# Kernel optimization log

Measured on AMD Instinct MI355X. Metric: run time of the kernel, lower is better.

Reference implementation:

```python
import jax, jax.numpy as jnp
import numpy as np

D_MODEL = 1024
N_HEADS = 16
HEAD_DIM = D_MODEL // N_HEADS


def setup_inputs() -> dict:
    key = jax.random.key(0)
    k1, k2, k3 = jax.random.split(key, 3)
    B, T = 4, 2048
    x = jax.random.normal(k1, (B, T, D_MODEL), dtype=jnp.float32)
    # match nn.Linear default init scale roughly (small weights for stability)
    w_qkv = jax.random.normal(k2, (D_MODEL, 3 * D_MODEL), dtype=jnp.float32) / np.sqrt(D_MODEL)
    w_proj = jax.random.normal(k3, (D_MODEL, D_MODEL), dtype=jnp.float32) / np.sqrt(D_MODEL)
    b_proj = jnp.zeros((D_MODEL,), dtype=jnp.float32)
    return {"x": x, "w_qkv": w_qkv, "w_proj": w_proj, "b_proj": b_proj}


def reference(x, w_qkv, w_proj, b_proj):
    B, T, C = x.shape
    qkv = x @ w_qkv  # [B,T,3C]
    q, k, v = jnp.split(qkv, 3, axis=-1)
    # [B, H, T, hd]
    q = q.reshape(B, T, N_HEADS, HEAD_DIM).transpose(0, 2, 1, 3)
    k = k.reshape(B, T, N_HEADS, HEAD_DIM).transpose(0, 2, 1, 3)
    v = v.reshape(B, T, N_HEADS, HEAD_DIM).transpose(0, 2, 1, 3)
    scale = 1.0 / np.sqrt(HEAD_DIM).astype(np.float32)
    att = jnp.einsum("bhqd,bhkd->bhqk", q, k) * scale
    causal = jnp.tril(jnp.ones((T, T), dtype=bool))
    att = jnp.where(causal[None, None], att, jnp.float32(-jnp.inf))
    att = jax.nn.softmax(att, axis=-1)
    # dropout p=0.0 (eval) -> identity
    out = jnp.einsum("bhqk,bhkd->bhqd", att, v)
    out = out.transpose(0, 2, 1, 3).reshape(B, T, C)
    return out @ w_proj + b_proj
```

## Files before the change

kernel.cpp:

```cpp
#include <hip/hip_runtime.h>
#include <stdint.h>

#define D_MODEL 1024
#define N_HEADS 16
#define HEAD_DIM 64
#define BATCH 4
#define SEQ 2048
#define ROWS (BATCH * SEQ)
#define K3 (3 * D_MODEL)
#define NQT (SEQ / 64)
#define SCALE_Q 0.1803368867f

typedef unsigned short u16;
typedef unsigned int u32;
typedef __attribute__((ext_vector_type(8))) short short8;
typedef __attribute__((ext_vector_type(4))) float floatx4;

typedef const __attribute__((address_space(1))) u32* gptr_t;
typedef __attribute__((address_space(3))) u32* lptr_t;

__device__ __forceinline__ unsigned cvt_pk(float lo, float hi) {
    unsigned r;
    asm("v_cvt_pk_bf16_f32 %0, %1, %2" : "=v"(r) : "v"(lo), "v"(hi));
    return r;
}

__global__ __launch_bounds__(256) void conv_f2b4(const float* __restrict__ x,
                                                 u16* __restrict__ xb, int n4) {
    int i = blockIdx.x * 256 + threadIdx.x;
    if (i < n4) {
        float4 v = ((const float4*)x)[i];
        uint2 p;
        p.x = cvt_pk(v.x, v.y);
        p.y = cvt_pk(v.z, v.w);
        ((uint2*)xb)[i] = p;
    }
}

__global__ __launch_bounds__(256) void transpose_f2b_t(const float* __restrict__ w,
                                                       u16* __restrict__ wt,
                                                       int R, int C) {
    __shared__ u16 tile[64][65];
    const int tx = threadIdx.x & 63;
    const int ty = threadIdx.x >> 6;
    const int r0 = blockIdx.y * 64, c0 = blockIdx.x * 64;
    #pragma unroll
    for (int i = 0; i < 16; i += 2) {
        const float a = w[(size_t)(r0 + i * 4 + ty) * C + c0 + tx];
        const float b = w[(size_t)(r0 + (i + 1) * 4 + ty) * C + c0 + tx];
        const unsigned p = cvt_pk(a, b);
        tile[i * 4 + ty][tx] = (u16)p;
        tile[(i + 1) * 4 + ty][tx] = (u16)(p >> 16);
    }
    __syncthreads();
    #pragma unroll
    for (int i = 0; i < 16; ++i) {
        const int c = i * 4 + ty;
        wt[(size_t)(c0 + c) * R + r0 + tx] = tile[tx][c];
    }
}

__global__ __launch_bounds__(256) void transpose_v2(const u16* __restrict__ v,
                                                    u16* __restrict__ vt) {
    __shared__ u16 tile[64][65];
    const int bh = blockIdx.y;
    const int t0 = blockIdx.x * 64;
    const int tx = threadIdx.x & 63, ty = threadIdx.x >> 6;
    const u16* src = v + ((size_t)bh * SEQ + t0) * HEAD_DIM;
    #pragma unroll
    for (int i = 0; i < 16; ++i) {
        const int r = i * 4 + ty;
        tile[r][tx] = src[r * HEAD_DIM + tx];
    }
    __syncthreads();
    u16* dst = vt + (size_t)bh * HEAD_DIM * SEQ + t0;
    #pragma unroll
    for (int i = 0; i < 16; ++i) {
        const int d = i * 4 + ty;
        dst[(size_t)d * SEQ + tx] = tile[tx][d];
    }
}

#define GEMM_CORE_GLD(KDIM, NXB)                                               \
    __shared__ u16 As[128][64];                                                \
    __shared__ u16 Bs[128][64];                                                \
    const int tid  = threadIdx.x;                                              \
    const int wave = tid >> 6, lane = tid & 63;                                \
    const int quad = lane >> 4, l15 = lane & 15;                               \
    const int wr = wave >> 1, wc = wave & 1;                                   \
    const int bid = (int)(blockIdx.y * gridDim.x + blockIdx.x);                \
    const int nwg = (int)(gridDim.x * gridDim.y);                              \
    const int swz = (bid & 7) * (nwg >> 3) + (bid >> 3);      \
    const int m0 = (swz / (NXB)) * 128, n0 = (swz % (NXB)) * 128;              \
    const int lrow8 = lane >> 3;                                               \
    const int csw = 8 * ((lane & 7) ^ lrow8);           \
    const int swA = (l15 & 7) * 8;                      \
    floatx4 acc[4][4] = {};                                                    \
    for (int k0 = 0; k0 < (KDIM); k0 += 64) {                                  \
        _Pragma("unroll")                                                      \
        for (int i = 0; i < 4; ++i) {                                          \
            const int rb = i * 32 + wave * 8;                                  \
            const int r  = rb + lrow8;                                         \
            __builtin_amdgcn_global_load_lds(                                  \
                (gptr_t)(A + (size_t)(m0 + r) * (KDIM) + k0 + csw),            \
                (lptr_t)(&As[rb][0]), 16, 0, 0);                               \
            __builtin_amdgcn_global_load_lds(                                  \
                (gptr_t)(Bt + (size_t)(n0 + r) * (KDIM) + k0 + csw),           \
                (lptr_t)(&Bs[rb][0]), 16, 0, 0);                               \
        }                                                                      \
        __syncthreads();                                                       \
        _Pragma("unroll")                                                      \
        for (int ks = 0; ks < 2; ++ks) {                                       \
            const int kk = ks * 32 + quad * 8;                                 \
            short8 af[4], bf[4];                                               \
            _Pragma("unroll")                                                  \
            for (int t = 0; t < 4; ++t) {                                      \
                af[t] = *(const short8*)&As[wr * 64 + t * 16 + l15][kk ^ swA]; \
                bf[t] = *(const short8*)&Bs[wc * 64 + t * 16 + l15][kk ^ swA]; \
            }                                                                  \
            _Pragma("unroll")                                                  \
            for (int i = 0; i < 4; ++i)                                        \
                _Pragma("unroll")                                              \
                for (int j = 0; j < 4; ++j)                                    \
                    acc[i][j] = __builtin_amdgcn_mfma_f32_16x16x32_bf16(       \
                        af[i], bf[j], acc[i][j], 0, 0, 0);                     \
        }                                                                      \
        __syncthreads();                                                       \
    }

__global__ __launch_bounds__(256) void gemm_qkv(const u16* __restrict__ A,
                                                const u16* __restrict__ Bt,
                                                u16* __restrict__ qo,
                                                u16* __restrict__ ko,
                                                u16* __restrict__ vo) {
    GEMM_CORE_GLD(D_MODEL, 24)
    const int which = n0 >> 10;
    u16* dst = which == 0 ? qo : (which == 1 ? ko : vo);
    const float scl = which == 0 ? SCALE_Q : 1.f;
    #pragma unroll
    for (int i = 0; i < 4; ++i)
        #pragma unroll
        for (int j = 0; j < 4; ++j) {
            const int col = n0 + wc * 64 + j * 16 + l15;
            const int rb  = m0 + wr * 64 + i * 16 + quad * 4;
            const int cc  = col & 1023;
            const int h = cc >> 6, d = cc & 63;
            #pragma unroll
            for (int rr = 0; rr < 4; rr += 2) {
                const unsigned pw = cvt_pk(acc[i][j][rr] * scl,
                                           acc[i][j][rr + 1] * scl);
                int row = rb + rr;
                int b_ = row >> 11, t_ = row & 2047;
                dst[(((size_t)(b_ * N_HEADS + h)) * SEQ + t_) * HEAD_DIM + d] =
                    (u16)pw;
                row = rb + rr + 1;
                b_ = row >> 11; t_ = row & 2047;
                dst[(((size_t)(b_ * N_HEADS + h)) * SEQ + t_) * HEAD_DIM + d] =
                    (u16)(pw >> 16);
            }
        }
}

__global__ __launch_bounds__(256) void gemm_proj(const u16* __restrict__ A,
                                                 const u16* __restrict__ Bt,
                                                 const float* __restrict__ bias,
                                                 float* __restrict__ out) {
    GEMM_CORE_GLD(D_MODEL, 8)
    #pragma unroll
    for (int i = 0; i < 4; ++i)
        #pragma unroll
        for (int j = 0; j < 4; ++j) {
            const int col = n0 + wc * 64 + j * 16 + l15;
            const int rb  = m0 + wr * 64 + i * 16 + quad * 4;
            const float bv = bias[col];
            #pragma unroll
            for (int rr = 0; rr < 4; ++rr) {
                const int row = rb + rr;
                out[(size_t)row * D_MODEL + col] = acc[i][j][rr] + bv;
            }
        }
}

__global__ __launch_bounds__(256, 4) void attn_mfma(const u16* __restrict__ q,
                                                    const u16* __restrict__ k,
                                                    const u16* __restrict__ vt,
                                                    u16* __restrict__ o) {
    __shared__ u16 Ks[2][64][64];
    __shared__ u16 Vs[2][64][64];
    __shared__ u16 Plds[4][16][64];
    const int tid = threadIdx.x;
    const int w = tid >> 6, lane = tid & 63;
    const int quad = lane >> 4, l15 = lane & 15;
    const int bid = (int)(blockIdx.y * 16 + blockIdx.x);
    const int swzb = (bid & 7) * 128 + (bid >> 3);
    const int bh = swzb >> 4;
    const int qx = swzb & 15;
    const int b = bh >> 4, h = bh & 15;
    const u16* kb  = k  + (size_t)bh * SEQ * HEAD_DIM;
    const u16* vtb = vt + (size_t)bh * HEAD_DIM * SEQ;
    const int lrow8 = lane >> 3;
    const int csw = 8 * ((lane & 7) ^ lrow8);
    const int swA = (l15 & 7) * 8;
    const int r0 = w * 16 + lrow8;
    const short8 ones = {0x3F80, 0x3F80, 0x3F80, 0x3F80,
                         0x3F80, 0x3F80, 0x3F80, 0x3F80};

    #pragma unroll 1
    for (int seg = 0; seg < 2; ++seg) {
        const int qt = seg ? qx : (NQT - 1 - qx);
        const int qrow = qt * 64 + w * 16 + l15;
        const u16* qp = q + ((size_t)bh * SEQ + qrow) * HEAD_DIM + quad * 8;
        const short8 bq0 = *(const short8*)(qp);
        const short8 bq1 = *(const short8*)(qp + 32);

        floatx4 O[4] = {};
        floatx4 Lacc = {};

        __syncthreads();
        __builtin_amdgcn_global_load_lds(
            (gptr_t)(kb + (size_t)(r0) * HEAD_DIM + csw),
            (lptr_t)(&Ks[0][w * 16][0]), 16, 0, 0);
        __builtin_amdgcn_global_load_lds(
            (gptr_t)(kb + (size_t)(r0 + 8) * HEAD_DIM + csw),
            (lptr_t)(&Ks[0][w * 16 + 8][0]), 16, 0, 0);
        __builtin_amdgcn_global_load_lds(
            (gptr_t)(vtb + (size_t)(r0) * SEQ + csw),
            (lptr_t)(&Vs[0][w * 16][0]), 16, 0, 0);
        __builtin_amdgcn_global_load_lds(
            (gptr_t)(vtb + (size_t)(r0 + 8) * SEQ + csw),
            (lptr_t)(&Vs[0][w * 16 + 8][0]), 16, 0, 0);

        for (int c = 0; c <= qt; ++c) {
            const int cb = c & 1;
            __syncthreads();
            if (c < qt) {
                const int nb = cb ^ 1;
                __builtin_amdgcn_global_load_lds(
                    (gptr_t)(kb + (size_t)((c + 1) * 64 + r0) * HEAD_DIM + csw),
                    (lptr_t)(&Ks[nb][w * 16][0]), 16, 0, 0);
                __builtin_amdgcn_global_load_lds(
                    (gptr_t)(kb + (size_t)((c + 1) * 64 + r0 + 8) * HEAD_DIM + csw),
                    (lptr_t)(&Ks[nb][w * 16 + 8][0]), 16, 0, 0);
                __builtin_amdgcn_global_load_lds(
                    (gptr_t)(vtb + (size_t)(r0) * SEQ + (c + 1) * 64 + csw),
                    (lptr_t)(&Vs[nb][w * 16][0]), 16, 0, 0);
                __builtin_amdgcn_global_load_lds(
                    (gptr_t)(vtb + (size_t)(r0 + 8) * SEQ + (c + 1) * 64 + csw),
                    (lptr_t)(&Vs[nb][w * 16 + 8][0]), 16, 0, 0);
            }
            floatx4 s[4];
            #pragma unroll
            for (int kt = 0; kt < 4; ++kt) {
                short8 ak0 = *(const short8*)&Ks[cb][kt * 16 + l15][(quad * 8) ^ swA];
                short8 ak1 = *(const short8*)&Ks[cb][kt * 16 + l15][(32 + quad * 8) ^ swA];
                floatx4 z = {};
                z = __builtin_amdgcn_mfma_f32_16x16x32_bf16(ak0, bq0, z, 0, 0, 0);
                z = __builtin_amdgcn_mfma_f32_16x16x32_bf16(ak1, bq1, z, 0, 0, 0);
                s[kt] = z;
            }
            float e[4][4];
            #pragma unroll
            for (int kt = 0; kt < 4; ++kt)
                #pragma unroll
                for (int r = 0; r < 4; ++r)
                    e[kt][r] = exp2f(s[kt][r]);
            if (c == qt) {
                #pragma unroll
                for (int kt = 0; kt < 4; ++kt)
                    #pragma unroll
                    for (int r = 0; r < 4; ++r)
                        if (kt * 16 + quad * 4 + r > w * 16 + l15) e[kt][r] = 0.f;
            }
            #pragma unroll
            for (int kt = 0; kt < 4; ++kt) {
                uint2 pkv;
                pkv.x = cvt_pk(e[kt][0], e[kt][1]);
                pkv.y = cvt_pk(e[kt][2], e[kt][3]);
                *(uint2*)&Plds[w][l15][(kt * 16 + quad * 4) ^ swA] = pkv;
            }
            short8 pb0 = *(const short8*)&Plds[w][l15][(quad * 8) ^ swA];
            short8 pb1 = *(const short8*)&Plds[w][l15][(32 + quad * 8) ^ swA];
            #pragma unroll
            for (int dt = 0; dt < 4; ++dt) {
                short8 av0 = *(const short8*)&Vs[cb][dt * 16 + l15][(quad * 8) ^ swA];
                short8 av1 = *(const short8*)&Vs[cb][dt * 16 + l15][(32 + quad * 8) ^ swA];
                O[dt] = __builtin_amdgcn_mfma_f32_16x16x32_bf16(av0, pb0, O[dt], 0, 0, 0);
                O[dt] = __builtin_amdgcn_mfma_f32_16x16x32_bf16(av1, pb1, O[dt], 0, 0, 0);
            }
            Lacc = __builtin_amdgcn_mfma_f32_16x16x32_bf16(ones, pb0, Lacc, 0, 0, 0);
            Lacc = __builtin_amdgcn_mfma_f32_16x16x32_bf16(ones, pb1, Lacc, 0, 0, 0);
        }
        const float inv = 1.f / Lacc[0];
        u16* op = o + ((size_t)(b * SEQ + qrow)) * D_MODEL + h * 64 + quad * 4;
        #pragma unroll
        for (int dt = 0; dt < 4; ++dt) {
            uint2 pkv;
            pkv.x = cvt_pk(O[dt][0] * inv, O[dt][1] * inv);
            pkv.y = cvt_pk(O[dt][2] * inv, O[dt][3] * inv);
            *(uint2*)(op + dt * 16) = pkv;
        }
    }
}

extern "C" void kernel_launch(void* const* d_in, const int* in_sizes, int n_in,
                              void* d_out, int out_size, void* d_ws, size_t ws_size,
                              hipStream_t stream) {
    const float* x      = (const float*)d_in[0];
    const float* w_qkv  = (const float*)d_in[1];
    const float* w_proj = (const float*)d_in[2];
    const float* b_proj = (const float*)d_in[3];
    float* out = (float*)d_out;

    u16* xb      = (u16*)d_ws;
    u16* wt_qkv  = xb + (size_t)ROWS * D_MODEL;
    u16* wt_proj = wt_qkv + (size_t)D_MODEL * K3;
    u16* qws     = wt_proj + (size_t)D_MODEL * D_MODEL;
    u16* kws     = qws + (size_t)ROWS * D_MODEL;
    u16* vtws    = kws + (size_t)ROWS * D_MODEL;
    u16* aout    = vtws + (size_t)ROWS * D_MODEL;
    u16* vnat    = aout;

    conv_f2b4<<<(ROWS * D_MODEL / 4 + 255) / 256, 256, 0, stream>>>(x, xb, ROWS * D_MODEL / 4);
    transpose_f2b_t<<<dim3(K3 / 64, D_MODEL / 64), 256, 0, stream>>>(w_qkv, wt_qkv, D_MODEL, K3);
    transpose_f2b_t<<<dim3(D_MODEL / 64, D_MODEL / 64), 256, 0, stream>>>(w_proj, wt_proj, D_MODEL, D_MODEL);

    gemm_qkv<<<dim3(K3 / 128, ROWS / 128), 256, 0, stream>>>(xb, wt_qkv, qws, kws, vnat);

    transpose_v2<<<dim3(SEQ / 64, BATCH * N_HEADS), 256, 0, stream>>>(vnat, vtws);

    attn_mfma<<<dim3(NQT / 2, BATCH * N_HEADS), 256, 0, stream>>>(qws, kws, vtws, aout);

    gemm_proj<<<dim3(D_MODEL / 128, ROWS / 128), 256, 0, stream>>>(aout, wt_proj, b_proj, out);
}
```

Measured before the change: 254.6 us.

## Fuse prep kernels, write V transposed from QKV GEMM, add MFMA priority

Merges the x bf16 conversion and both weight transposes into a single launch that dispatches on block index. The QKV GEMM epilogue now transposes V tiles through swizzled shared memory and writes V^T directly, removing the separate transpose kernel and its round trip through global memory. The attention loop raises wave priority with s_setprio around MFMA sections so matrix instructions are issued ahead of other waves' work. Risks: the prep kernel uses hard-coded block counts, the V epilogue adds an extra barrier and LDS traffic, and setprio may reduce overlap.

```diff
diff --git a/kernel.cpp b/kernel.cpp
--- a/kernel.cpp
+++ b/kernel.cpp
@@ -25,25 +25,39 @@
     return r;
 }
 
-__global__ __launch_bounds__(256) void conv_f2b4(const float* __restrict__ x,
-                                                 u16* __restrict__ xb, int n4) {
-    int i = blockIdx.x * 256 + threadIdx.x;
-    if (i < n4) {
+__global__ __launch_bounds__(256) void prep_fused(const float* __restrict__ x,
+                                                  u16* __restrict__ xb,
+                                                  const float* __restrict__ w_qkv,
+                                                  u16* __restrict__ wt_qkv,
+                                                  const float* __restrict__ w_proj,
+                                                  u16* __restrict__ wt_proj) {
+    __shared__ u16 tile[64][65];
+    const int bid = blockIdx.x;
+    if (bid < 8192) {
+        const int i = bid * 256 + threadIdx.x;
         float4 v = ((const float4*)x)[i];
         uint2 p;
         p.x = cvt_pk(v.x, v.y);
         p.y = cvt_pk(v.z, v.w);
         ((uint2*)xb)[i] = p;
-    }
-}
-
-__global__ __launch_bounds__(256) void transpose_f2b_t(const float* __restrict__ w,
-                                                       u16* __restrict__ wt,
-                                                       int R, int C) {
-    __shared__ u16 tile[64][65];
+        return;
+    }
+    const float* w;
+    u16* wt;
+    int C, bx, by;
+    if (bid < 8192 + 768) {
+        const int r = bid - 8192;
+        w = w_qkv; wt = wt_qkv; C = K3;
+        bx = r % 48; by = r / 48;
+    } else {
+        const int r = bid - 8960;
+        w = w_proj; wt = wt_proj; C = D_MODEL;
+        bx = r & 15; by = r >> 4;
+    }
+    const int R = D_MODEL;
     const int tx = threadIdx.x & 63;
     const int ty = threadIdx.x >> 6;
-    const int r0 = blockIdx.y * 64, c0 = blockIdx.x * 64;
+    const int r0 = by * 64, c0 = bx * 64;
     #pragma unroll
     for (int i = 0; i < 16; i += 2) {
         const float a = w[(size_t)(r0 + i * 4 + ty) * C + c0 + tx];
@@ -60,30 +74,10 @@
     }
 }
 
-__global__ __launch_bounds__(256) void transpose_v2(const u16* __restrict__ v,
-                                                    u16* __restrict__ vt) {
-    __shared__ u16 tile[64][65];
-    const int bh = blockIdx.y;
-    const int t0 = blockIdx.x * 64;
-    const int tx = threadIdx.x & 63, ty = threadIdx.x >> 6;
-    const u16* src = v + ((size_t)bh * SEQ + t0) * HEAD_DIM;
-    #pragma unroll
-    for (int i = 0; i < 16; ++i) {
-        const int r = i * 4 + ty;
-        tile[r][tx] = src[r * HEAD_DIM + tx];
-    }
-    __syncthreads();
-    u16* dst = vt + (size_t)bh * HEAD_DIM * SEQ + t0;
-    #pragma unroll
-    for (int i = 0; i < 16; ++i) {
-        const int d = i * 4 + ty;
-        dst[(size_t)d * SEQ + tx] = tile[tx][d];
-    }
-}
-
 #define GEMM_CORE_GLD(KDIM, NXB)                                               \
-    __shared__ u16 As[128][64];                                                \
-    __shared__ u16 Bs[128][64];                                                \
+    __shared__ u16 SM[2][128][64];                                             \
+    u16 (*As)[64] = SM[0];                                                     \
+    u16 (*Bs)[64] = SM[1];                                                     \
     const int tid  = threadIdx.x;                                              \
     const int wave = tid >> 6, lane = tid & 63;                                \
     const int quad = lane >> 4, l15 = lane & 15;                               \
@@ -132,10 +126,41 @@
                                                 const u16* __restrict__ Bt,
                                                 u16* __restrict__ qo,
                                                 u16* __restrict__ ko,
-                                                u16* __restrict__ vo) {
+                                                u16* __restrict__ vt) {
     GEMM_CORE_GLD(D_MODEL, 24)
     const int which = n0 >> 10;
-    u16* dst = which == 0 ? qo : (which == 1 ? ko : vo);
+    if (which == 2) {
+        char* Tv = (char*)&SM[wc][0][0];
+        #pragma unroll
+        for (int i = 0; i < 4; ++i) {
+            const int tb = wr * 64 + i * 16 + quad * 4;
+            #pragma unroll
+            for (int j = 0; j < 4; ++j) {
+                const int d = j * 16 + l15;
+                const unsigned xo = (unsigned)((d & 7) << 5);
+                char* base = Tv + d * 256;
+                *(u32*)(base + (((tb + 0) * 2) ^ xo)) =
+                    cvt_pk(acc[i][j][0], acc[i][j][1]);
+                *(u32*)(base + (((tb + 2) * 2) ^ xo)) =
+                    cvt_pk(acc[i][j][2], acc[i][j][3]);
+            }
+        }
+        __syncthreads();
+        const int idx = wr * 64 + lane;
+        const int d = idx >> 1, tb2 = (idx & 1) * 64;
+        const int b_ = m0 >> 11, t0 = m0 & 2047;
+        const int h = ((n0 - 2048) >> 6) + wc;
+        u16* dst = vt + ((size_t)(b_ * N_HEADS + h) * HEAD_DIM + d) * SEQ + t0 + tb2;
+        const char* src = (const char*)&SM[wc][0][0] + d * 256;
+        const unsigned xo = (unsigned)((d & 7) << 5);
+        #pragma unroll
+        for (int c8 = 0; c8 < 8; ++c8) {
+            const uint4 vv = *(const uint4*)(src + (((tb2 + c8 * 8) * 2) ^ xo));
+            *(uint4*)(dst + c8 * 8) = vv;
+        }
+        return;
+    }
+    u16* dst = which == 0 ? qo : ko;
     const float scl = which == 0 ? SCALE_Q : 1.f;
     #pragma unroll
     for (int i = 0; i < 4; ++i)
@@ -254,8 +279,10 @@
                 short8 ak0 = *(const short8*)&Ks[cb][kt * 16 + l15][(quad * 8) ^ swA];
                 short8 ak1 = *(const short8*)&Ks[cb][kt * 16 + l15][(32 + quad * 8) ^ swA];
                 floatx4 z = {};
+                __builtin_amdgcn_s_setprio(1);
                 z = __builtin_amdgcn_mfma_f32_16x16x32_bf16(ak0, bq0, z, 0, 0, 0);
                 z = __builtin_amdgcn_mfma_f32_16x16x32_bf16(ak1, bq1, z, 0, 0, 0);
+                __builtin_amdgcn_s_setprio(0);
                 s[kt] = z;
             }
             float e[4][4];
@@ -280,6 +307,7 @@
             }
             short8 pb0 = *(const short8*)&Plds[w][l15][(quad * 8) ^ swA];
             short8 pb1 = *(const short8*)&Plds[w][l15][(32 + quad * 8) ^ swA];
+            __builtin_amdgcn_s_setprio(1);
             #pragma unroll
             for (int dt = 0; dt < 4; ++dt) {
                 short8 av0 = *(const short8*)&Vs[cb][dt * 16 + l15][(quad * 8) ^ swA];
@@ -289,6 +317,7 @@
             }
             Lacc = __builtin_amdgcn_mfma_f32_16x16x32_bf16(ones, pb0, Lacc, 0, 0, 0);
             Lacc = __builtin_amdgcn_mfma_f32_16x16x32_bf16(ones, pb1, Lacc, 0, 0, 0);
+            __builtin_amdgcn_s_setprio(0);
         }
         const float inv = 1.f / Lacc[0];
         u16* op = o + ((size_t)(b * SEQ + qrow)) * D_MODEL + h * 64 + quad * 4;
@@ -318,15 +347,11 @@
     u16* kws     = qws + (size_t)ROWS * D_MODEL;
     u16* vtws    = kws + (size_t)ROWS * D_MODEL;
     u16* aout    = vtws + (size_t)ROWS * D_MODEL;
-    u16* vnat    = aout;
-
-    conv_f2b4<<<(ROWS * D_MODEL / 4 + 255) / 256, 256, 0, stream>>>(x, xb, ROWS * D_MODEL / 4);
-    transpose_f2b_t<<<dim3(K3 / 64, D_MODEL / 64), 256, 0, stream>>>(w_qkv, wt_qkv, D_MODEL, K3);
-    transpose_f2b_t<<<dim3(D_MODEL / 64, D_MODEL / 64), 256, 0, stream>>>(w_proj, wt_proj, D_MODEL, D_MODEL);
-
-    gemm_qkv<<<dim3(K3 / 128, ROWS / 128), 256, 0, stream>>>(xb, wt_qkv, qws, kws, vnat);
-
-    transpose_v2<<<dim3(SEQ / 64, BATCH * N_HEADS), 256, 0, stream>>>(vnat, vtws);
+
+    prep_fused<<<8192 + 768 + 256, 256, 0, stream>>>(x, xb, w_qkv, wt_qkv,
+                                                     w_proj, wt_proj);
+
+    gemm_qkv<<<dim3(K3 / 128, ROWS / 128), 256, 0, stream>>>(xb, wt_qkv, qws, kws, vtws);
 
     attn_mfma<<<dim3(NQT / 2, BATCH * N_HEADS), 256, 0, stream>>>(qws, kws, vtws, aout);
 
```

Result: slower. 263.2 us (+3.4%).

## Fuse prep kernels, double-buffer QKV GEMM loads, raise MFMA priority in attention

Applied to the files above, without the earlier changes.

Merges the three bf16 conversion and transpose kernels into a single launch that dispatches on block index, removing two launch gaps. Rewrites the QKV GEMM with a two-stage LDS double buffer, so global-to-LDS loads for the next K tile are in flight during the current tile's MFMAs, with explicit vmcnt waits and barriers. Wraps the attention MFMA sections in s_setprio to favour matrix issue across waves. The costs are double the LDS in the QKV GEMM, which may lower occupancy, and hand-tuned wait counts that must match the number of issued loads.

```diff
diff --git a/kernel.cpp b/kernel.cpp
--- a/kernel.cpp
+++ b/kernel.cpp
@@ -25,25 +25,39 @@
     return r;
 }
 
-__global__ __launch_bounds__(256) void conv_f2b4(const float* __restrict__ x,
-                                                 u16* __restrict__ xb, int n4) {
-    int i = blockIdx.x * 256 + threadIdx.x;
-    if (i < n4) {
+__global__ __launch_bounds__(256) void prep_fused(const float* __restrict__ x,
+                                                  u16* __restrict__ xb,
+                                                  const float* __restrict__ w_qkv,
+                                                  u16* __restrict__ wt_qkv,
+                                                  const float* __restrict__ w_proj,
+                                                  u16* __restrict__ wt_proj) {
+    __shared__ u16 tile[64][65];
+    const int bid = blockIdx.x;
+    if (bid < 8192) {
+        const int i = bid * 256 + threadIdx.x;
         float4 v = ((const float4*)x)[i];
         uint2 p;
         p.x = cvt_pk(v.x, v.y);
         p.y = cvt_pk(v.z, v.w);
         ((uint2*)xb)[i] = p;
-    }
-}
-
-__global__ __launch_bounds__(256) void transpose_f2b_t(const float* __restrict__ w,
-                                                       u16* __restrict__ wt,
-                                                       int R, int C) {
-    __shared__ u16 tile[64][65];
+        return;
+    }
+    const float* w;
+    u16* wt;
+    int C, bx, by;
+    if (bid < 8192 + 768) {
+        const int r = bid - 8192;
+        w = w_qkv; wt = wt_qkv; C = K3;
+        bx = r % 48; by = r / 48;
+    } else {
+        const int r = bid - 8960;
+        w = w_proj; wt = wt_proj; C = D_MODEL;
+        bx = r & 15; by = r >> 4;
+    }
+    const int R = D_MODEL;
     const int tx = threadIdx.x & 63;
     const int ty = threadIdx.x >> 6;
-    const int r0 = blockIdx.y * 64, c0 = blockIdx.x * 64;
+    const int r0 = by * 64, c0 = bx * 64;
     #pragma unroll
     for (int i = 0; i < 16; i += 2) {
         const float a = w[(size_t)(r0 + i * 4 + ty) * C + c0 + tx];
@@ -79,6 +93,111 @@
         const int d = i * 4 + ty;
         dst[(size_t)d * SEQ + tx] = tile[tx][d];
     }
+}
+
+__global__ __launch_bounds__(256) void gemm_qkv(const u16* __restrict__ A,
+                                                const u16* __restrict__ Bt,
+                                                u16* __restrict__ qo,
+                                                u16* __restrict__ ko,
+                                                u16* __restrict__ vo) {
+    __shared__ u16 As[2][128][64];
+    __shared__ u16 Bs[2][128][64];
+    const int tid  = threadIdx.x;
+    const int wave = tid >> 6, lane = tid & 63;
+    const int quad = lane >> 4, l15 = lane & 15;
+    const int wr = wave >> 1, wc = wave & 1;
+    const int bid = (int)(blockIdx.y * gridDim.x + blockIdx.x);
+    const int nwg = (int)(gridDim.x * gridDim.y);
+    const int swz = (bid & 7) * (nwg >> 3) + (bid >> 3);
+    const int m0 = (swz / 24) * 128, n0 = (swz % 24) * 128;
+    const int lrow8 = lane >> 3;
+    const int csw = 8 * ((lane & 7) ^ lrow8);
+    const int swA = (l15 & 7) * 8;
+    floatx4 acc[4][4] = {};
+    const u16* Ab = A  + (size_t)m0 * D_MODEL + csw;
+    const u16* Bb = Bt + (size_t)n0 * D_MODEL + csw;
+
+#define QKV_ISSUE8(buf, k0)                                                    \
+    _Pragma("unroll")                                                          \
+    for (int i = 0; i < 4; ++i) {                                              \
+        const int rb = i * 32 + wave * 8;                                      \
+        __builtin_amdgcn_global_load_lds(                                      \
+            (gptr_t)(Ab + (size_t)(rb + lrow8) * D_MODEL + (k0)),              \
+            (lptr_t)(&As[buf][rb][0]), 16, 0, 0);                              \
+        __builtin_amdgcn_global_load_lds(                                      \
+            (gptr_t)(Bb + (size_t)(rb + lrow8) * D_MODEL + (k0)),              \
+            (lptr_t)(&Bs[buf][rb][0]), 16, 0, 0);                              \
+    }
+
+#define QKV_COMPUTE(buf)                                                       \
+    _Pragma("unroll")                                                          \
+    for (int ks = 0; ks < 2; ++ks) {                                           \
+        const int kk = ks * 32 + quad * 8;                                     \
+        short8 af[4], bf[4];                                                   \
+        _Pragma("unroll")                                                      \
+        for (int t2 = 0; t2 < 4; ++t2) {                                       \
+            af[t2] = *(const short8*)&As[buf][wr * 64 + t2 * 16 + l15][kk ^ swA]; \
+            bf[t2] = *(const short8*)&Bs[buf][wc * 64 + t2 * 16 + l15][kk ^ swA]; \
+        }                                                                      \
+        _Pragma("unroll")                                                      \
+        for (int i = 0; i < 4; ++i)                                            \
+            _Pragma("unroll")                                                  \
+            for (int j = 0; j < 4; ++j)                                        \
+                acc[i][j] = __builtin_amdgcn_mfma_f32_16x16x32_bf16(           \
+                    af[i], bf[j], acc[i][j], 0, 0, 0);                         \
+    }
+
+#define WAITV8 do { asm volatile("s_waitcnt vmcnt(8)" ::: "memory");           \
+                    __builtin_amdgcn_sched_barrier(0); } while (0)
+#define WAITV0 do { asm volatile("s_waitcnt vmcnt(0)" ::: "memory");           \
+                    __builtin_amdgcn_sched_barrier(0); } while (0)
+#define BARR   do { __builtin_amdgcn_s_barrier();                              \
+                    __builtin_amdgcn_sched_barrier(0); } while (0)
+
+    QKV_ISSUE8(0, 0)
+    #pragma unroll 1
+    for (int t = 0; t < 14; t += 2) {
+        QKV_ISSUE8(1, (t + 1) * 64)
+        WAITV8; BARR;
+        QKV_COMPUTE(0)
+        BARR;
+        QKV_ISSUE8(0, (t + 2) * 64)
+        WAITV8; BARR;
+        QKV_COMPUTE(1)
+        BARR;
+    }
+    QKV_ISSUE8(1, 15 * 64)
+    WAITV8; BARR;
+    QKV_COMPUTE(0)
+    BARR;
+    WAITV0; BARR;
+    QKV_COMPUTE(1)
+
+    const int which = n0 >> 10;
+    u16* dst = which == 0 ? qo : (which == 1 ? ko : vo);
+    const float scl = which == 0 ? SCALE_Q : 1.f;
+    #pragma unroll
+    for (int i = 0; i < 4; ++i)
+        #pragma unroll
+        for (int j = 0; j < 4; ++j) {
+            const int col = n0 + wc * 64 + j * 16 + l15;
+            const int rb  = m0 + wr * 64 + i * 16 + quad * 4;
+            const int cc  = col & 1023;
+            const int h = cc >> 6, d = cc & 63;
+            #pragma unroll
+            for (int rr = 0; rr < 4; rr += 2) {
+                const unsigned pw = cvt_pk(acc[i][j][rr] * scl,
+                                           acc[i][j][rr + 1] * scl);
+                int row = rb + rr;
+                int b_ = row >> 11, t_ = row & 2047;
+                dst[(((size_t)(b_ * N_HEADS + h)) * SEQ + t_) * HEAD_DIM + d] =
+                    (u16)pw;
+                row = rb + rr + 1;
+                b_ = row >> 11; t_ = row & 2047;
+                dst[(((size_t)(b_ * N_HEADS + h)) * SEQ + t_) * HEAD_DIM + d] =
+                    (u16)(pw >> 16);
+            }
+        }
 }
 
 #define GEMM_CORE_GLD(KDIM, NXB)                                               \
@@ -128,39 +247,6 @@
         __syncthreads();                                                       \
     }
 
-__global__ __launch_bounds__(256) void gemm_qkv(const u16* __restrict__ A,
-                                                const u16* __restrict__ Bt,
-                                                u16* __restrict__ qo,
-                                                u16* __restrict__ ko,
-                                                u16* __restrict__ vo) {
-    GEMM_CORE_GLD(D_MODEL, 24)
-    const int which = n0 >> 10;
-    u16* dst = which == 0 ? qo : (which == 1 ? ko : vo);
-    const float scl = which == 0 ? SCALE_Q : 1.f;
-    #pragma unroll
-    for (int i = 0; i < 4; ++i)
-        #pragma unroll
-        for (int j = 0; j < 4; ++j) {
-            const int col = n0 + wc * 64 + j * 16 + l15;
-            const int rb  = m0 + wr * 64 + i * 16 + quad * 4;
-            const int cc  = col & 1023;
-            const int h = cc >> 6, d = cc & 63;
-            #pragma unroll
-            for (int rr = 0; rr < 4; rr += 2) {
-                const unsigned pw = cvt_pk(acc[i][j][rr] * scl,
-                                           acc[i][j][rr + 1] * scl);
-                int row = rb + rr;
-                int b_ = row >> 11, t_ = row & 2047;
-                dst[(((size_t)(b_ * N_HEADS + h)) * SEQ + t_) * HEAD_DIM + d] =
-                    (u16)pw;
-                row = rb + rr + 1;
-                b_ = row >> 11; t_ = row & 2047;
-                dst[(((size_t)(b_ * N_HEADS + h)) * SEQ + t_) * HEAD_DIM + d] =
-                    (u16)(pw >> 16);
-            }
-        }
-}
-
 __global__ __launch_bounds__(256) void gemm_proj(const u16* __restrict__ A,
                                                  const u16* __restrict__ Bt,
                                                  const float* __restrict__ bias,
@@ -254,8 +340,10 @@
                 short8 ak0 = *(const short8*)&Ks[cb][kt * 16 + l15][(quad * 8) ^ swA];
                 short8 ak1 = *(const short8*)&Ks[cb][kt * 16 + l15][(32 + quad * 8) ^ swA];
                 floatx4 z = {};
+                __builtin_amdgcn_s_setprio(1);
                 z = __builtin_amdgcn_mfma_f32_16x16x32_bf16(ak0, bq0, z, 0, 0, 0);
                 z = __builtin_amdgcn_mfma_f32_16x16x32_bf16(ak1, bq1, z, 0, 0, 0);
+                __builtin_amdgcn_s_setprio(0);
                 s[kt] = z;
             }
             float e[4][4];
@@ -280,6 +368,7 @@
             }
             short8 pb0 = *(const short8*)&Plds[w][l15][(quad * 8) ^ swA];
             short8 pb1 = *(const short8*)&Plds[w][l15][(32 + quad * 8) ^ swA];
+            __builtin_amdgcn_s_setprio(1);
             #pragma unroll
             for (int dt = 0; dt < 4; ++dt) {
                 short8 av0 = *(const short8*)&Vs[cb][dt * 16 + l15][(quad * 8) ^ swA];
@@ -289,6 +378,7 @@
             }
             Lacc = __builtin_amdgcn_mfma_f32_16x16x32_bf16(ones, pb0, Lacc, 0, 0, 0);
             Lacc = __builtin_amdgcn_mfma_f32_16x16x32_bf16(ones, pb1, Lacc, 0, 0, 0);
+            __builtin_amdgcn_s_setprio(0);
         }
         const float inv = 1.f / Lacc[0];
         u16* op = o + ((size_t)(b * SEQ + qrow)) * D_MODEL + h * 64 + quad * 4;
@@ -320,9 +410,8 @@
     u16* aout    = vtws + (size_t)ROWS * D_MODEL;
     u16* vnat    = aout;
 
-    conv_f2b4<<<(ROWS * D_MODEL / 4 + 255) / 256, 256, 0, stream>>>(x, xb, ROWS * D_MODEL / 4);
-    transpose_f2b_t<<<dim3(K3 / 64, D_MODEL / 64), 256, 0, stream>>>(w_qkv, wt_qkv, D_MODEL, K3);
-    transpose_f2b_t<<<dim3(D_MODEL / 64, D_MODEL / 64), 256, 0, stream>>>(w_proj, wt_proj, D_MODEL, D_MODEL);
+    prep_fused<<<8192 + 768 + 256, 256, 0, stream>>>(x, xb, w_qkv, wt_qkv,
+                                                     w_proj, wt_proj);
 
     gemm_qkv<<<dim3(K3 / 128, ROWS / 128), 256, 0, stream>>>(xb, wt_qkv, qws, kws, vnat);
 
```

New measurement: 251.8 us. No clear change (-1.1%).
